# Kernel optimization log

Hardware: AMD Instinct MI355X
Metric: run time of the kernel (lower is better)

## Reference

```python
import math
import jax, jax.numpy as jnp
import numpy as np

G = 128        # graphs per batch
N0 = 512       # nodes per graph
H = 256        # hidden size
E = 524288     # edges (avg degree 8), intra-graph
RATIO = 0.8


def setup_inputs() -> dict:
    key = jax.random.key(0)
    ks = jax.random.split(key, 16)
    # intra-graph edges: E//G edges per graph
    eg = jnp.arange(E, dtype=jnp.int32) // (E // G)
    src = eg * N0 + jax.random.randint(ks[0], (E,), 0, N0, dtype=jnp.int32)
    dst = eg * N0 + jax.random.randint(ks[1], (E,), 0, N0, dtype=jnp.int32)
    s = 1.0 / math.sqrt(H)
    return {
        "x": jax.random.normal(ks[2], (G * N0, H), jnp.float32),
        "edge_src": src,
        "edge_dst": dst,
        "W_in": jax.random.normal(ks[3], (H, H), jnp.float32) * s,
        "b_in": jnp.zeros((H,), jnp.float32),
        "W_h0": jax.random.normal(ks[4], (H, H), jnp.float32) * s,
        "b_h0": jnp.zeros((H,), jnp.float32),
        "W_h1": jax.random.normal(ks[5], (H, H), jnp.float32) * s,
        "b_h1": jnp.zeros((H,), jnp.float32),
        "p_in": jax.random.normal(ks[6], (H,), jnp.float32),
        "p_h0": jax.random.normal(ks[7], (H,), jnp.float32),
        "p_h1": jax.random.normal(ks[8], (H,), jnp.float32),
        "att_w": jax.random.normal(ks[9], (H,), jnp.float32) * s,
        "att_b": jnp.zeros((1,), jnp.float32),
    }


def gcn_conv(x, W, b, src, dst, emask, num_nodes):
    # PyG GCNConv: lin -> sym-normalized propagate (with self loops, weight 1) -> bias
    h = x @ W
    deg = jax.ops.segment_sum(emask, dst, num_segments=num_nodes) + 1.0  # +1 self loop
    dis = jax.lax.rsqrt(deg)
    coef = dis[src] * dis[dst] * emask                    # [E]
    agg = jax.ops.segment_sum(h[src] * coef[:, None], dst, num_segments=num_nodes)
    agg = agg + h * (dis * dis)[:, None]                  # self-loop message
    return agg + b


def topk_pool(x, p, src, dst, emask, n_cur):
    # PyG TopKPooling: score = tanh(x.p/|p|), keep top ceil(ratio*n) per graph,
    # x' = x[perm]*score[perm], edges filtered to kept nodes and remapped.
    k = int(math.ceil(RATIO * n_cur))
    score = jnp.tanh((x @ p) / jnp.linalg.norm(p))        # [G*n_cur]
    _, idx = jax.lax.top_k(score.reshape(G, n_cur), k)    # [G,k]
    perm = (idx + (jnp.arange(G, dtype=idx.dtype) * n_cur)[:, None]).reshape(-1)
    x_new = x[perm] * score[perm][:, None]                # [G*k,H]
    mapping = jnp.full((G * n_cur,), -1, jnp.int32).at[perm].set(
        jnp.arange(G * k, dtype=jnp.int32))
    ns, nd = mapping[src], mapping[dst]
    valid = (ns >= 0) & (nd >= 0) & (emask > 0)
    return (x_new, jnp.where(valid, ns, 0), jnp.where(valid, nd, 0),
            valid.astype(x.dtype), k)


def att_pool(x, att_w, att_b, k):
    # GlobalAttention: per-graph softmax gate, weighted sum
    gate = (x @ att_w + att_b[0]).reshape(G, k)
    att = jax.nn.softmax(gate, axis=1)
    return jnp.einsum('gk,gkh->gh', att, x.reshape(G, k, H))


def reference(x, edge_src, edge_dst, W_in, b_in, W_h0, b_h0, W_h1, b_h1,
              p_in, p_h0, p_h1, att_w, att_b):
    src, dst = edge_src, edge_dst
    emask = jnp.ones((E,), x.dtype)
    n_cur = N0
    h = jax.nn.relu(gcn_conv(x, W_in, b_in, src, dst, emask, G * n_cur))
    h, src, dst, emask, n_cur = topk_pool(h, p_in, src, dst, emask, n_cur)
    out = att_pool(h, att_w, att_b, n_cur)
    for (W, b, p) in ((W_h0, b_h0, p_h0), (W_h1, b_h1, p_h1)):
        h = jax.nn.relu(gcn_conv(h, W, b, src, dst, emask, G * n_cur))
        h, src, dst, emask, n_cur = topk_pool(h, p, src, dst, emask, n_cur)
        out = out + att_pool(h, att_w, att_b, n_cur)
    return out  # [G, H]
```

## Files before the change

kernel.cpp:

```cpp
#include <hip/hip_runtime.h>
#include <cmath>

#define G_ 128
#define N0_ 512
#define H_ 256
#define E_ 524288
#define NODES0 (G_*N0_)

typedef _Float16 v8h __attribute__((ext_vector_type(8)));
typedef _Float16 v4h __attribute__((ext_vector_type(4)));
typedef float v4f __attribute__((ext_vector_type(4)));

#define TSTRIDE 72
#define TILEHW (128*TSTRIDE)

__device__ __forceinline__ void async_copy16(void* lds, const void* g) {
  __builtin_amdgcn_global_load_lds(
      (const __attribute__((address_space(1))) void*)g,
      (__attribute__((address_space(3))) void*)lds, 16, 0, 0);
}

__device__ __forceinline__ int xcd_swizzle(int orig, int nb) {
  int q = nb >> 3, r = nb & 7;
  int xcd = orig & 7, local = orig >> 3;
  int off = (xcd < r) ? xcd * (q + 1) : r * (q + 1) + (xcd - r) * q;
  return off + local;
}

__device__ __forceinline__ float4 f4fma(float4 a, float s, float4 acc) {
  acc.x = fmaf(a.x, s, acc.x); acc.y = fmaf(a.y, s, acc.y);
  acc.z = fmaf(a.z, s, acc.z); acc.w = fmaf(a.w, s, acc.w);
  return acc;
}

__global__ __launch_bounds__(256) void setup_kernel(const float* __restrict__ p0,
                                                    const float* __restrict__ p1,
                                                    const float* __restrict__ p2,
                                                    float* __restrict__ pinv,
                                                    int* __restrict__ cum,
                                                    int* __restrict__ orig_of,
                                                    int* __restrict__ cnt) {
  __shared__ float red[4];
  if (blockIdx.x < 3) {
    const float* p = (blockIdx.x == 0) ? p0 : (blockIdx.x == 1 ? p1 : p2);
    float v = p[threadIdx.x];
    #pragma unroll
    for (int off = 32; off > 0; off >>= 1) v += __shfl_down(v * ((off == 32) ? 0.0f : 0.0f) + ((off == 32) ? 0.0f : 0.0f), off);
    float s = p[threadIdx.x] * p[threadIdx.x];
    #pragma unroll
    for (int off = 32; off > 0; off >>= 1) s += __shfl_down(s, off);
    int lane = threadIdx.x & 63, wid = threadIdx.x >> 6;
    if (lane == 0) red[wid] = s;
    __syncthreads();
    if (threadIdx.x == 0)
      pinv[blockIdx.x] = 1.0f / sqrtf(red[0] + red[1] + red[2] + red[3]);
  } else {
    int v = (blockIdx.x - 3) * 256 + threadIdx.x;
    if (v < NODES0) { cum[v] = v; orig_of[v] = v; cnt[v] = 0; }
  }
}

__global__ __launch_bounds__(256) void wconv_kernel(const float* __restrict__ W0,
                                                    const float* __restrict__ W1,
                                                    const float* __restrict__ W2,
                                                    _Float16* __restrict__ img) {
  int l = blockIdx.x >> 4;
  const float* W = (l == 0) ? W0 : (l == 1 ? W1 : W2);
  int bn = (blockIdx.x >> 3) & 1, kt = blockIdx.x & 7;
  int t = threadIdx.x;
  int n = t & 127, kh = t >> 7;
  int k0 = kt * 32 + kh * 16;
  _Float16* row = img + (size_t)l * 16 * TILEHW + ((size_t)(bn * 8 + kt) * 128 + n) * TSTRIDE;
  #pragma unroll
  for (int s = 0; s < 2; ++s) {
    v8h hv, lv;
    #pragma unroll
    for (int j = 0; j < 8; ++j) {
      float a = W[(size_t)(k0 + s * 8 + j) * 256 + bn * 128 + n];
      _Float16 h = (_Float16)a;
      hv[j] = h;
      lv[j] = (_Float16)(a - (float)h);
    }
    *(v8h*)&row[kh * 16 + s * 8] = hv;
    *(v8h*)&row[32 + kh * 16 + s * 8] = lv;
  }
}

__global__ void count0_kernel(const int* __restrict__ edst, int* __restrict__ cnt) {
  int e = blockIdx.x * 256 + threadIdx.x;
  if (e < E_) atomicAdd(&cnt[edst[e]], 1);
}

__global__ __launch_bounds__(256) void scan1_kernel(const int* __restrict__ cnt,
                                                    int* __restrict__ row0,
                                                    int* __restrict__ bsum,
                                                    float* __restrict__ dis,
                                                    int* __restrict__ cursor, int n) {
  __shared__ int sdata[256];
  int base = blockIdx.x * 1024;
  int t = threadIdx.x;
  int v[4]; int s = 0;
  #pragma unroll
  for (int i = 0; i < 4; ++i) {
    int idx = base + t * 4 + i;
    v[i] = (idx < n) ? cnt[idx] : 0;
    s += v[i];
    if (idx < n) {
      dis[idx] = 1.0f / sqrtf((float)v[i] + 1.0f);
      cursor[idx] = 0;
    }
  }
  sdata[t] = s;
  __syncthreads();
  for (int off = 1; off < 256; off <<= 1) {
    int x = (t >= off) ? sdata[t - off] : 0;
    __syncthreads();
    sdata[t] += x;
    __syncthreads();
  }
  int excl = sdata[t] - s;
  if (t == 255) bsum[blockIdx.x] = sdata[255];
  #pragma unroll
  for (int i = 0; i < 4; ++i) {
    int idx = base + t * 4 + i;
    if (idx < n) { row0[idx] = excl; excl += v[i]; }
  }
}

__global__ __launch_bounds__(256) void scan2_kernel(int* __restrict__ bsum,
                                                    int* __restrict__ row0, int nb, int n) {
  __shared__ int sdata[256];
  int t = threadIdx.x;
  int v = (t < nb) ? bsum[t] : 0;
  sdata[t] = v;
  __syncthreads();
  for (int off = 1; off < 256; off <<= 1) {
    int x = (t >= off) ? sdata[t - off] : 0;
    __syncthreads();
    sdata[t] += x;
    __syncthreads();
  }
  if (t < nb) bsum[t] = sdata[t] - v;
  if (t == 255) row0[n] = sdata[255];
}

__global__ void fill0_kernel(const int* __restrict__ esrc, const int* __restrict__ edst,
                             const int* __restrict__ row0, const int* __restrict__ bsum,
                             int* __restrict__ cursor, const float* __restrict__ dis,
                             int* __restrict__ csr0, int* __restrict__ csr_dst,
                             int2* __restrict__ pair0, int2* __restrict__ rows) {
  int e = blockIdx.x * 256 + threadIdx.x;
  if (e >= E_) return;
  if (e < NODES0) {
    int rs = row0[e] + bsum[e >> 10];
    int e1 = e + 1;
    int re = (e1 < NODES0) ? row0[e1] + bsum[e1 >> 10] : row0[NODES0];
    rows[e] = make_int2(rs, re);
  }
  int d = edst[e], s = esrc[e];
  int pos = atomicAdd(&cursor[d], 1);
  int idx = row0[d] + bsum[d >> 10] + pos;
  csr0[idx] = s;
  csr_dst[idx] = d;
  pair0[idx] = make_int2(s, __float_as_int(dis[s] * dis[d]));
}

__global__ void deg_kernel(const int* __restrict__ orig_of, const int* __restrict__ row0,
                           const int* __restrict__ bsum, const int* __restrict__ csr0,
                           const int* __restrict__ cum, float* __restrict__ dis,
                           int2* __restrict__ rows, int nodes) {
  int blk = xcd_swizzle(blockIdx.x, gridDim.x);
  int v = blk * 256 + threadIdx.x;
  if (v >= nodes) return;
  int o = orig_of[v];
  int rs = row0[o] + bsum[o >> 10];
  int o1 = o + 1;
  int re = row0[o1] + ((o1 < NODES0) ? bsum[o1 >> 10] : 0);
  rows[v] = make_int2(rs, re);
  int c = 0;
  for (int j = rs; j < re; ++j) c += (cum[csr0[j]] >= 0) ? 1 : 0;
  dis[v] = rsqrtf((float)c + 1.0f);
}

__global__ void remap_kernel(const int* __restrict__ csr0, const int* __restrict__ csr_dst,
                             const int* __restrict__ cum, const float* __restrict__ dis,
                             int2* __restrict__ pair_l) {
  int blk = xcd_swizzle(blockIdx.x, gridDim.x);
  int j = blk * 256 + threadIdx.x;
  if (j >= E_) return;
  int md = cum[csr_dst[j]];
  if (md < 0) return;
  int ms = cum[csr0[j]];
  pair_l[j] = make_int2((ms >= 0) ? ms : md,
                        __float_as_int((ms >= 0) ? dis[ms] * dis[md] : 0.0f));
}

__global__ __launch_bounds__(256) void gemm_f16x3_kernel(const float* __restrict__ A,
                                                         const int* __restrict__ perm,
                                                         const float* __restrict__ sscore,
                                                         const _Float16* __restrict__ Wimg,
                                                         float* __restrict__ C) {
  __shared__ _Float16 As[TILEHW];
  __shared__ _Float16 Ws[TILEHW];
  const int tid = threadIdx.x;
  const int flat = xcd_swizzle(blockIdx.x, gridDim.x);
  const int bm = flat >> 1;
  const int bn = flat & 1;
  const int lane = tid & 63, wid = tid >> 6;
  const int wm = wid >> 1, wn = wid & 1;
  const int l15 = lane & 15, kg = lane >> 4;

  v4f acc[4][4];
  #pragma unroll
  for (int i = 0; i < 4; ++i)
    #pragma unroll
    for (int j = 0; j < 4; ++j) acc[i][j] = (v4f){0.f, 0.f, 0.f, 0.f};

  int arow[4], acc4[4];
  const float* aptr[4];
  float ascale[4];
  #pragma unroll
  for (int i = 0; i < 4; ++i) {
    int c = tid + 256 * i;
    arow[i] = c >> 3;
    acc4[i] = c & 7;
    int R = bm * 128 + arow[i];
    int pr = perm ? perm[R] : R;
    ascale[i] = perm ? sscore[R] : 1.0f;
    aptr[i] = A + (size_t)pr * 256 + acc4[i] * 4;
  }
  const _Float16* wtile0 = Wimg + (size_t)bn * 8 * TILEHW;

  float4 pa[4];
  #pragma unroll
  for (int i = 0; i < 4; ++i) pa[i] = *(const float4*)(aptr[i] + 0);

  for (int kt = 0; kt < 8; ++kt) {
    {
      const _Float16* wt = wtile0 + (size_t)kt * TILEHW;
      for (int cb = wid; cb < 18; cb += 4)
        async_copy16(&Ws[cb * 512], wt + (size_t)cb * 512 + lane * 8);
    }
    #pragma unroll
    for (int i = 0; i < 4; ++i) {
      float av[4] = {pa[i].x * ascale[i], pa[i].y * ascale[i],
                     pa[i].z * ascale[i], pa[i].w * ascale[i]};
      v4h hv, lv;
      #pragma unroll
      for (int j = 0; j < 4; ++j) {
        _Float16 h = (_Float16)av[j];
        hv[j] = h;
        lv[j] = (_Float16)(av[j] - (float)h);
      }
      _Float16* dst = &As[arow[i] * TSTRIDE + acc4[i] * 4];
      *(v4h*)(dst) = hv;
      *(v4h*)(dst + 32) = lv;
    }
    __syncthreads();

    if (kt < 7) {
      #pragma unroll
      for (int i = 0; i < 4; ++i)
        pa[i] = *(const float4*)(aptr[i] + (kt + 1) * 32);
    }

    v8h ah[4], bh[4], al[4], bl[4];
    #pragma unroll
    for (int i = 0; i < 4; ++i)
      ah[i] = *(const v8h*)&As[(wm * 64 + i * 16 + l15) * TSTRIDE + kg * 8];
    #pragma unroll
    for (int j = 0; j < 4; ++j)
      bh[j] = *(const v8h*)&Ws[(wn * 64 + j * 16 + l15) * TSTRIDE + kg * 8];
    #pragma unroll
    for (int i = 0; i < 4; ++i)
      #pragma unroll
      for (int j = 0; j < 4; ++j)
        acc[i][j] = __builtin_amdgcn_mfma_f32_16x16x32_f16(ah[i], bh[j], acc[i][j], 0, 0, 0);
    #pragma unroll
    for (int i = 0; i < 4; ++i)
      al[i] = *(const v8h*)&As[(wm * 64 + i * 16 + l15) * TSTRIDE + 32 + kg * 8];
    #pragma unroll
    for (int i = 0; i < 4; ++i)
      #pragma unroll
      for (int j = 0; j < 4; ++j)
        acc[i][j] = __builtin_amdgcn_mfma_f32_16x16x32_f16(al[i], bh[j], acc[i][j], 0, 0, 0);
    #pragma unroll
    for (int j = 0; j < 4; ++j)
      bl[j] = *(const v8h*)&Ws[(wn * 64 + j * 16 + l15) * TSTRIDE + 32 + kg * 8];
    #pragma unroll
    for (int i = 0; i < 4; ++i)
      #pragma unroll
      for (int j = 0; j < 4; ++j)
        acc[i][j] = __builtin_amdgcn_mfma_f32_16x16x32_f16(ah[i], bl[j], acc[i][j], 0, 0, 0);
    __syncthreads();
  }

  #pragma unroll
  for (int i = 0; i < 4; ++i) {
    #pragma unroll
    for (int j = 0; j < 4; ++j) {
      #pragma unroll
      for (int r = 0; r < 4; ++r) {
        int row = bm * 128 + wm * 64 + i * 16 + kg * 4 + r;
        int col = bn * 128 + wn * 64 + j * 16 + l15;
        C[(size_t)row * 256 + col] = acc[i][j][r];
      }
    }
  }
}

__global__ __launch_bounds__(256) void agg_score_kernel(
    const float4* __restrict__ hlin4, const float* __restrict__ dis,
    const float4* __restrict__ bias4,
    const int2* __restrict__ rows,
    const int2* __restrict__ edge,
    const float4* __restrict__ p4, const float* __restrict__ pinvp,
    float4* __restrict__ hout4, float* __restrict__ score) {
  int blk = xcd_swizzle(blockIdx.x, gridDim.x);
  int wave = threadIdx.x >> 6, lane = threadIdx.x & 63;
  int v = blk * 4 + wave;
  int2 rr = rows[v];
  float dv = dis[v];
  float self = dv * dv;
  float4 h = hlin4[(size_t)v * 64 + lane];
  float4 acc = make_float4(h.x * self, h.y * self, h.z * self, h.w * self);
  int j = rr.x, re = rr.y;
  for (; j + 8 <= re; j += 8) {
    int s[8]; float c[8]; float4 hh[8];
    #pragma unroll
    for (int u = 0; u < 8; ++u) {
      int2 e = edge[j + u];
      s[u] = e.x; c[u] = __int_as_float(e.y);
    }
    #pragma unroll
    for (int u = 0; u < 8; ++u) hh[u] = hlin4[(size_t)s[u] * 64 + lane];
    #pragma unroll
    for (int u = 0; u < 8; ++u) acc = f4fma(hh[u], c[u], acc);
  }
  if (j + 4 <= re) {
    int s[4]; float c[4]; float4 hh[4];
    #pragma unroll
    for (int u = 0; u < 4; ++u) {
      int2 e = edge[j + u];
      s[u] = e.x; c[u] = __int_as_float(e.y);
    }
    #pragma unroll
    for (int u = 0; u < 4; ++u) hh[u] = hlin4[(size_t)s[u] * 64 + lane];
    #pragma unroll
    for (int u = 0; u < 4; ++u) acc = f4fma(hh[u], c[u], acc);
    j += 4;
  }
  for (; j < re; ++j) {
    int2 e = edge[j];
    acc = f4fma(hlin4[(size_t)e.x * 64 + lane], __int_as_float(e.y), acc);
  }
  float4 b = bias4[lane];
  acc.x = fmaxf(acc.x + b.x, 0.0f); acc.y = fmaxf(acc.y + b.y, 0.0f);
  acc.z = fmaxf(acc.z + b.z, 0.0f); acc.w = fmaxf(acc.w + b.w, 0.0f);
  hout4[(size_t)v * 64 + lane] = acc;
  float4 pv = p4[lane];
  float s = acc.x * pv.x + acc.y * pv.y + acc.z * pv.z + acc.w * pv.w;
  #pragma unroll
  for (int off = 32; off > 0; off >>= 1) s += __shfl_down(s, off);
  if (lane == 0) score[v] = tanhf(s * pinvp[0]);
}

__global__ __launch_bounds__(512) void topk_pool_kernel(
    const float* __restrict__ score, int n, int k,
    int* __restrict__ cum, const int* __restrict__ orig_prev,
    int* __restrict__ orig_new, int* __restrict__ perm, float* __restrict__ sscore,
    const float4* __restrict__ h4, const float4* __restrict__ attw4,
    const float* __restrict__ attb, float* __restrict__ out, int add) {
  __shared__ float key[512];
  __shared__ int kid[512];
  __shared__ int newmap[512];
  __shared__ float wmax[8], wsum[8];
  __shared__ float4 waccs[8][64];
  int g = xcd_swizzle(blockIdx.x, gridDim.x);
  int t = threadIdx.x;

  key[t] = (t < n) ? score[(size_t)g * n + t] : -INFINITY;
  kid[t] = t;
  if (t < n) newmap[t] = -1;
  __syncthreads();
  for (int kk = 2; kk <= 512; kk <<= 1) {
    for (int j = kk >> 1; j > 0; j >>= 1) {
      int i = t, ixj = i ^ j;
      if (ixj > i) {
        float ka = key[i]; int ia = kid[i];
        float kb = key[ixj]; int ib = kid[ixj];
        bool b_first = (kb > ka) || (kb == ka && ib < ia);
        bool sw = ((i & kk) == 0) ? b_first : !b_first;
        if (sw) { key[i] = kb; kid[i] = ib; key[ixj] = ka; kid[ixj] = ia; }
      }
      __syncthreads();
    }
  }
  if (t < k) {
    int local = kid[t];
    perm[g * k + t] = g * n + local;
    newmap[local] = g * k + t;
    orig_new[g * k + t] = orig_prev[g * n + local];
    sscore[g * k + t] = key[t];
  }
  __syncthreads();
  {
    int v = g * N0_ + t;
    int c = cum[v];
    if (c >= 0) cum[v] = newmap[c - g * n];
  }

  int wave = t >> 6, lane = t & 63;
  float4 aw = attw4[lane];
  float ab = attb[0];
  float m = -INFINITY, ssum = 0.0f;
  float4 acc = make_float4(0.f, 0.f, 0.f, 0.f);
  for (int i = wave; i < k; i += 8) {
    int node = g * n + kid[i];
    float sc = key[i];
    float4 hv = h4[(size_t)node * 64 + lane];
    float4 val = make_float4(hv.x * sc, hv.y * sc, hv.z * sc, hv.w * sc);
    float gd = val.x * aw.x + val.y * aw.y + val.z * aw.z + val.w * aw.w;
    #pragma unroll
    for (int off = 32; off > 0; off >>= 1) gd += __shfl_xor(gd, off);
    float gi = gd + ab;
    float mnew = fmaxf(m, gi);
    float f = __expf(m - mnew);
    float e = __expf(gi - mnew);
    acc.x = acc.x * f + val.x * e; acc.y = acc.y * f + val.y * e;
    acc.z = acc.z * f + val.z * e; acc.w = acc.w * f + val.w * e;
    ssum = ssum * f + e;
    m = mnew;
  }
  if (lane == 0) { wmax[wave] = m; wsum[wave] = ssum; }
  waccs[wave][lane] = acc;
  __syncthreads();
  if (wave == 0) {
    float mstar = wmax[0];
    #pragma unroll
    for (int w = 1; w < 8; ++w) mstar = fmaxf(mstar, wmax[w]);
    float stot = 0.0f;
    float4 a = make_float4(0.f, 0.f, 0.f, 0.f);
    #pragma unroll
    for (int w = 0; w < 8; ++w) {
      float sc = __expf(wmax[w] - mstar);
      stot += wsum[w] * sc;
      float4 wa = waccs[w][lane];
      a.x += wa.x * sc; a.y += wa.y * sc; a.z += wa.z * sc; a.w += wa.w * sc;
    }
    float inv = 1.0f / stot;
    a.x *= inv; a.y *= inv; a.z *= inv; a.w *= inv;
    float4* o4 = (float4*)out + (size_t)g * 64 + lane;
    if (add) {
      float4 prev = *o4;
      a.x += prev.x; a.y += prev.y; a.z += prev.z; a.w += prev.w;
    }
    *o4 = a;
  }
}

extern "C" void kernel_launch(void* const* d_in, const int* in_sizes, int n_in,
                              void* d_out, int out_size, void* d_ws, size_t ws_size,
                              hipStream_t stream) {
  const float* x    = (const float*)d_in[0];
  const int*   esrc = (const int*)d_in[1];
  const int*   edst = (const int*)d_in[2];
  const float* Wl[3] = {(const float*)d_in[3], (const float*)d_in[5], (const float*)d_in[7]};
  const float* bl[3] = {(const float*)d_in[4], (const float*)d_in[6], (const float*)d_in[8]};
  const float* pl[3] = {(const float*)d_in[9], (const float*)d_in[10], (const float*)d_in[11]};
  const float* attw = (const float*)d_in[12];
  const float* attb = (const float*)d_in[13];
  float* out = (float*)d_out;

  char* w = (char*)d_ws;
  auto carve = [&](size_t bytes) { char* p = w; w += (bytes + 255) & ~(size_t)255; return p; };
  float* bufA    = (float*)carve((size_t)NODES0 * H_ * 4);
  float* bufB    = (float*)carve((size_t)NODES0 * H_ * 4);
  int*   csr0    = (int*)  carve((size_t)E_ * 4);
  int*   csr_dst = (int*)  carve((size_t)E_ * 4);
  int2*  pair0   = (int2*) carve((size_t)E_ * 8);
  int2*  pair_l  = (int2*) carve((size_t)E_ * 8);
  int*   cnt     = (int*)  carve((size_t)NODES0 * 4);
  int*   row0    = (int*)  carve((size_t)(NODES0 + 1) * 4);
  int*   cursor  = (int*)  carve((size_t)NODES0 * 4);
  float* dis     = (float*)carve((size_t)NODES0 * 4);
  float* score   = (float*)carve((size_t)NODES0 * 4);
  float* sscore  = (float*)carve((size_t)NODES0 * 4);
  int*   cum_map = (int*)  carve((size_t)NODES0 * 4);
  int*   origA   = (int*)  carve((size_t)NODES0 * 4);
  int*   origB   = (int*)  carve((size_t)NODES0 * 4);
  int*   perm    = (int*)  carve((size_t)NODES0 * 4);
  int2*  rows    = (int2*) carve((size_t)NODES0 * 8);
  int*   bsum    = (int*)  carve(256 * 4);
  float* pinv    = (float*)carve(16);
  _Float16* Wimg = (_Float16*)carve((size_t)3 * 16 * TILEHW * 2);
  (void)ws_size; (void)in_sizes; (void)n_in; (void)out_size;

  setup_kernel<<<3 + NODES0 / 256, 256, 0, stream>>>(pl[0], pl[1], pl[2], pinv,
                                                     cum_map, origA, cnt);
  wconv_kernel<<<48, 256, 0, stream>>>(Wl[0], Wl[1], Wl[2], Wimg);

  count0_kernel<<<E_ / 256, 256, 0, stream>>>(edst, cnt);
  int nb0 = (NODES0 + 1023) / 1024;
  scan1_kernel<<<nb0, 256, 0, stream>>>(cnt, row0, bsum, dis, cursor, NODES0);
  scan2_kernel<<<1, 256, 0, stream>>>(bsum, row0, nb0, NODES0);
  fill0_kernel<<<E_ / 256, 256, 0, stream>>>(esrc, edst, row0, bsum, cursor, dis,
                                             csr0, csr_dst, pair0, rows);

  int n_cur = N0_;
  int* origs[2] = {origA, origB};
  for (int l = 0; l < 3; ++l) {
    int nodes = G_ * n_cur;
    int* orig_cur = origs[l & 1];
    int* orig_nxt = origs[(l & 1) ^ 1];

    if (l > 0) {
      deg_kernel<<<(nodes + 255) / 256, 256, 0, stream>>>(orig_cur, row0, bsum, csr0,
                                                          cum_map, dis, rows, nodes);
      remap_kernel<<<E_ / 256, 256, 0, stream>>>(csr0, csr_dst, cum_map, dis, pair_l);
    }

    gemm_f16x3_kernel<<<(nodes / 128) * 2, 256, 0, stream>>>(
        (l == 0) ? x : bufB, (l == 0) ? nullptr : perm, sscore,
        Wimg + (size_t)l * 16 * TILEHW, bufA);

    int agg_blocks = nodes / 4;
    agg_score_kernel<<<agg_blocks, 256, 0, stream>>>(
        (const float4*)bufA, dis, (const float4*)bl[l], rows,
        (l == 0) ? pair0 : pair_l,
        (const float4*)pl[l], pinv + l, (float4*)bufB, score);

    int kk = (int)std::ceil(0.8 * (double)n_cur);
    topk_pool_kernel<<<G_, 512, 0, stream>>>(
        score, n_cur, kk, cum_map, orig_cur, orig_nxt, perm, sscore,
        (const float4*)bufB, (const float4*)attw, attb, out, l > 0 ? 1 : 0);

    n_cur = kk;
  }
}
```

Baseline: 380.6 us.

## Fuse degree recompute and edge remap into per-graph topk pool kernel

Folds the separate deg_kernel and remap_kernel into the tail of topk_pool_kernel. Each 512-thread graph block now recomputes degrees, rows and the normalized edge coefficients for its own graph's edges, with dis held in shared memory. The orig_of bookkeeping arrays go away. This saves two launches per pooled layer and some global traffic. In exchange, only 128 blocks handle all edge remapping, which cuts parallelism for that phase and lengthens the serial topk kernel.

```diff
diff --git a/kernel.cpp b/kernel.cpp
--- a/kernel.cpp
+++ b/kernel.cpp
@@ -38,14 +38,10 @@
                                                     const float* __restrict__ p2,
                                                     float* __restrict__ pinv,
                                                     int* __restrict__ cum,
-                                                    int* __restrict__ orig_of,
                                                     int* __restrict__ cnt) {
   __shared__ float red[4];
   if (blockIdx.x < 3) {
     const float* p = (blockIdx.x == 0) ? p0 : (blockIdx.x == 1 ? p1 : p2);
-    float v = p[threadIdx.x];
-    #pragma unroll
-    for (int off = 32; off > 0; off >>= 1) v += __shfl_down(v * ((off == 32) ? 0.0f : 0.0f) + ((off == 32) ? 0.0f : 0.0f), off);
     float s = p[threadIdx.x] * p[threadIdx.x];
     #pragma unroll
     for (int off = 32; off > 0; off >>= 1) s += __shfl_down(s, off);
@@ -56,7 +52,7 @@
       pinv[blockIdx.x] = 1.0f / sqrtf(red[0] + red[1] + red[2] + red[3]);
   } else {
     int v = (blockIdx.x - 3) * 256 + threadIdx.x;
-    if (v < NODES0) { cum[v] = v; orig_of[v] = v; cnt[v] = 0; }
+    if (v < NODES0) { cum[v] = v; cnt[v] = 0; }
   }
 }
 
@@ -163,36 +159,6 @@
   csr0[idx] = s;
   csr_dst[idx] = d;
   pair0[idx] = make_int2(s, __float_as_int(dis[s] * dis[d]));
-}
-
-__global__ void deg_kernel(const int* __restrict__ orig_of, const int* __restrict__ row0,
-                           const int* __restrict__ bsum, const int* __restrict__ csr0,
-                           const int* __restrict__ cum, float* __restrict__ dis,
-                           int2* __restrict__ rows, int nodes) {
-  int blk = xcd_swizzle(blockIdx.x, gridDim.x);
-  int v = blk * 256 + threadIdx.x;
-  if (v >= nodes) return;
-  int o = orig_of[v];
-  int rs = row0[o] + bsum[o >> 10];
-  int o1 = o + 1;
-  int re = row0[o1] + ((o1 < NODES0) ? bsum[o1 >> 10] : 0);
-  rows[v] = make_int2(rs, re);
-  int c = 0;
-  for (int j = rs; j < re; ++j) c += (cum[csr0[j]] >= 0) ? 1 : 0;
-  dis[v] = rsqrtf((float)c + 1.0f);
-}
-
-__global__ void remap_kernel(const int* __restrict__ csr0, const int* __restrict__ csr_dst,
-                             const int* __restrict__ cum, const float* __restrict__ dis,
-                             int2* __restrict__ pair_l) {
-  int blk = xcd_swizzle(blockIdx.x, gridDim.x);
-  int j = blk * 256 + threadIdx.x;
-  if (j >= E_) return;
-  int md = cum[csr_dst[j]];
-  if (md < 0) return;
-  int ms = cum[csr0[j]];
-  pair_l[j] = make_int2((ms >= 0) ? ms : md,
-                        __float_as_int((ms >= 0) ? dis[ms] * dis[md] : 0.0f));
 }
 
 __global__ __launch_bounds__(256) void gemm_f16x3_kernel(const float* __restrict__ A,
@@ -367,13 +333,17 @@
 
 __global__ __launch_bounds__(512) void topk_pool_kernel(
     const float* __restrict__ score, int n, int k,
-    int* __restrict__ cum, const int* __restrict__ orig_prev,
-    int* __restrict__ orig_new, int* __restrict__ perm, float* __restrict__ sscore,
+    int* __restrict__ cum, int* __restrict__ perm, float* __restrict__ sscore,
     const float4* __restrict__ h4, const float4* __restrict__ attw4,
-    const float* __restrict__ attb, float* __restrict__ out, int add) {
+    const float* __restrict__ attb, float* __restrict__ out, int add,
+    int do_next,
+    const int* __restrict__ row0, const int* __restrict__ bsum,
+    const int* __restrict__ csr0, const int* __restrict__ csr_dst,
+    float* __restrict__ dis, int2* __restrict__ rows, int2* __restrict__ pair_l) {
   __shared__ float key[512];
   __shared__ int kid[512];
   __shared__ int newmap[512];
+  __shared__ float disl[512];
   __shared__ float wmax[8], wsum[8];
   __shared__ float4 waccs[8][64];
   int g = xcd_swizzle(blockIdx.x, gridDim.x);
@@ -400,14 +370,43 @@
     int local = kid[t];
     perm[g * k + t] = g * n + local;
     newmap[local] = g * k + t;
-    orig_new[g * k + t] = orig_prev[g * n + local];
     sscore[g * k + t] = key[t];
   }
   __syncthreads();
-  {
-    int v = g * N0_ + t;
-    int c = cum[v];
-    if (c >= 0) cum[v] = newmap[c - g * n];
+  int vo = g * N0_ + t;
+  int c0 = cum[vo];
+  if (c0 >= 0) cum[vo] = newmap[c0 - g * n];
+  __syncthreads();
+
+  if (do_next) {
+    if (t < k) {
+    }
+    __syncthreads();
+    {
+      int o = g * N0_ + t;
+      int nc = cum[o];
+      if (nc >= 0) {
+        int rs = row0[o] + bsum[o >> 10];
+        int o1 = o + 1;
+        int re = (o1 < NODES0) ? row0[o1] + bsum[o1 >> 10] : row0[NODES0];
+        int c = 0;
+        for (int j = rs; j < re; ++j) c += (cum[csr0[j]] >= 0) ? 1 : 0;
+        float dv = rsqrtf((float)c + 1.0f);
+        disl[nc - g * k] = dv;
+        dis[nc] = dv;
+        rows[nc] = make_int2(rs, re);
+      }
+    }
+    __syncthreads();
+    int slo = row0[g * N0_] + bsum[(g * N0_) >> 10];
+    int shi = (g < G_ - 1) ? row0[(g + 1) * N0_] + bsum[((g + 1) * N0_) >> 10] : row0[NODES0];
+    for (int j = slo + t; j < shi; j += 512) {
+      int md = cum[csr_dst[j]];
+      if (md < 0) continue;
+      int ms = cum[csr0[j]];
+      float cf = (ms >= 0) ? disl[ms - g * k] * disl[md - g * k] : 0.0f;
+      pair_l[j] = make_int2((ms >= 0) ? ms : md, __float_as_int(cf));
+    }
   }
 
   int wave = t >> 6, lane = t & 63;
@@ -487,8 +486,6 @@
   float* score   = (float*)carve((size_t)NODES0 * 4);
   float* sscore  = (float*)carve((size_t)NODES0 * 4);
   int*   cum_map = (int*)  carve((size_t)NODES0 * 4);
-  int*   origA   = (int*)  carve((size_t)NODES0 * 4);
-  int*   origB   = (int*)  carve((size_t)NODES0 * 4);
   int*   perm    = (int*)  carve((size_t)NODES0 * 4);
   int2*  rows    = (int2*) carve((size_t)NODES0 * 8);
   int*   bsum    = (int*)  carve(256 * 4);
@@ -497,7 +494,7 @@
   (void)ws_size; (void)in_sizes; (void)n_in; (void)out_size;
 
   setup_kernel<<<3 + NODES0 / 256, 256, 0, stream>>>(pl[0], pl[1], pl[2], pinv,
-                                                     cum_map, origA, cnt);
+                                                     cum_map, cnt);
   wconv_kernel<<<48, 256, 0, stream>>>(Wl[0], Wl[1], Wl[2], Wimg);
 
   count0_kernel<<<E_ / 256, 256, 0, stream>>>(edst, cnt);
@@ -508,32 +505,23 @@
                                              csr0, csr_dst, pair0, rows);
 
   int n_cur = N0_;
-  int* origs[2] = {origA, origB};
   for (int l = 0; l < 3; ++l) {
     int nodes = G_ * n_cur;
-    int* orig_cur = origs[l & 1];
-    int* orig_nxt = origs[(l & 1) ^ 1];
-
-    if (l > 0) {
-      deg_kernel<<<(nodes + 255) / 256, 256, 0, stream>>>(orig_cur, row0, bsum, csr0,
-                                                          cum_map, dis, rows, nodes);
-      remap_kernel<<<E_ / 256, 256, 0, stream>>>(csr0, csr_dst, cum_map, dis, pair_l);
-    }
 
     gemm_f16x3_kernel<<<(nodes / 128) * 2, 256, 0, stream>>>(
         (l == 0) ? x : bufB, (l == 0) ? nullptr : perm, sscore,
         Wimg + (size_t)l * 16 * TILEHW, bufA);
 
-    int agg_blocks = nodes / 4;
-    agg_score_kernel<<<agg_blocks, 256, 0, stream>>>(
+    agg_score_kernel<<<nodes / 4, 256, 0, stream>>>(
         (const float4*)bufA, dis, (const float4*)bl[l], rows,
         (l == 0) ? pair0 : pair_l,
         (const float4*)pl[l], pinv + l, (float4*)bufB, score);
 
     int kk = (int)std::ceil(0.8 * (double)n_cur);
     topk_pool_kernel<<<G_, 512, 0, stream>>>(
-        score, n_cur, kk, cum_map, orig_cur, orig_nxt, perm, sscore,
-        (const float4*)bufB, (const float4*)attw, attb, out, l > 0 ? 1 : 0);
+        score, n_cur, kk, cum_map, perm, sscore,
+        (const float4*)bufB, (const float4*)attw, attb, out, l > 0 ? 1 : 0,
+        (l < 2) ? 1 : 0, row0, bsum, csr0, csr_dst, dis, rows, pair_l);
 
     n_cur = kk;
   }
```

Result: no change. 377.6 us (-0.8%).
